# Performance work log

Measured on AMD Instinct MI355X. Metric: run time of the kernel, lower is better.

## Reference

```python
import jax, jax.numpy as jnp
import numpy as np

B = 16384  # batch size
DN = ('NCHW', 'OIHW', 'NCHW')


def maxpool2(x):
    # 2x2 max pool, stride 2, VALID (matches nn.MaxPool2d(2, 2))
    return jax.lax.reduce_window(x, -jnp.inf, jax.lax.max,
                                 (1, 1, 2, 2), (1, 1, 2, 2), 'VALID')


def setup_inputs() -> dict:
    key = jax.random.key(0)
    ks = jax.random.split(key, 7)
    return {
        'x': jax.random.normal(ks[0], (B, 1, 32, 32), jnp.float32),
        'w1': jax.random.normal(ks[1], (6, 1, 5, 5), jnp.float32) * 0.1,
        'w2': jax.random.normal(ks[2], (16, 6, 5, 5), jnp.float32) * 0.1,
        'fw1': jax.random.normal(ks[3], (120, 400), jnp.float32) * 0.05,
        'fw2': jax.random.normal(ks[4], (84, 120), jnp.float32) * 0.05,
        'fc3_w': jax.random.normal(ks[5], (10, 84), jnp.float32) * 0.1,
        'fc3_b': jax.random.normal(ks[6], (10,), jnp.float32) * 0.1,
    }


def reference(x, w1, w2, fw1, fw2, fc3_w, fc3_b):
    # conv1 (no bias in StdConv2D) -> relu -> pool
    h = jax.lax.conv_general_dilated(x, w1, (1, 1), 'VALID', dimension_numbers=DN)
    h = maxpool2(jax.nn.relu(h))                      # [B,6,14,14]
    # conv2 -> relu -> pool
    h = jax.lax.conv_general_dilated(h, w2, (1, 1), 'VALID', dimension_numbers=DN)
    h = maxpool2(jax.nn.relu(h))                      # [B,16,5,5]
    h = h.reshape(h.shape[0], 400)                    # channel-major flatten, as torch view
    # StdFC layers: x @ W.T, no bias
    h = jax.nn.relu(h @ fw1.T)                        # [B,120]
    h = jax.nn.relu(h @ fw2.T)                        # [B,84]
    logits = h @ fc3_w.T + fc3_b                      # nn.Linear fc3 with bias
    return jax.nn.softmax(logits, axis=1)
```

## Files before the change

kernel.cpp:

```cpp
#include <hip/hip_runtime.h>
#include <hip/hip_fp16.h>
#include <math.h>

#define TH 256

typedef __attribute__((ext_vector_type(8))) short short8;
typedef __attribute__((ext_vector_type(4))) float floatx4;

#define P1_S   0
#define X_S    9424
#define P2_S   9424
#define BT_S   12816
#define H1_S   12816
#define H2_S   13904
#define LOG_F  7368
#define W1B_U  7752
#define LDS_F  7904

static __device__ __forceinline__ unsigned short f2bf(float x) {
    union { float f; unsigned u; } v; v.f = x;
    return (unsigned short)((v.u + 0x7FFFu + ((v.u >> 16) & 1u)) >> 16);
}
static __device__ __forceinline__ __half2 uash2(unsigned u) {
    union { unsigned u; __half2 h; } v; v.u = u; return v.h;
}
static __device__ __forceinline__ unsigned bfpack(unsigned hi, unsigned lo) {
    return __builtin_amdgcn_perm(hi, lo, 0x07060302u);
}
static __device__ __forceinline__ short8 load_bf8t(const float* row, int kb, int K) {
    int b0 = (kb + 4 <= K) ? kb : (K - 8);
    int b1 = (kb + 8 <= K) ? (kb + 4) : (K - 8);
    uint4 w0 = *(const uint4*)(row + b0);
    uint4 w1 = *(const uint4*)(row + b1);
    union { int4 i; short8 s; } r;
    r.i.x = (int)bfpack(w0.y, w0.x);
    r.i.y = (int)bfpack(w0.w, w0.z);
    r.i.z = (int)bfpack(w1.y, w1.x);
    r.i.w = (int)bfpack(w1.w, w1.z);
    return r.s;
}

__global__ __launch_bounds__(TH) void lenet_kernel(
    const float* __restrict__ x,
    const float* __restrict__ w1,
    const float* __restrict__ w2g,
    const float* __restrict__ fw1,
    const float* __restrict__ fw2,
    const float* __restrict__ fc3w,
    const float* __restrict__ fc3b,
    float* __restrict__ out)
{
    __shared__ __align__(16) float sf[LDS_F];
    short* sh = (short*)sf;
    unsigned* su = (unsigned*)sf;
    const int* p1i = (const int*)sf;

    const int tid  = threadIdx.x;
    const int blk  = blockIdx.x;
    const int lane = tid & 63;
    const int wid  = tid >> 6;
    const int g    = lane >> 4;
    const int cn   = lane & 15;
    const int pr   = cn & 7;
    const int dyr  = cn >> 3;

    float4 xreg[3];
    {
        const float4* xg0 = (const float4*)(x + (size_t)blk * 8 * 1024);
        #pragma unroll
        for (int j = 0; j < 3; ++j) { int e = tid + j * TH; if (e < 768) xreg[j] = xg0[e]; }
    }
    for (int sub = 0; sub < 3; ++sub) {
        const int nimg = (sub < 2) ? 3 : 2;
        if (sub) __syncthreads();
        #pragma unroll
        for (int j = 0; j < 3; ++j) {
            int e = tid + j * TH;
            if (e < nimg * 256) {
                float4 v = xreg[j];
                int m = e >> 8, rem = e & 255;
                int y = rem >> 3, k4 = rem & 7;
                int off = X_S + m * 1090 + y * 34 + k4 * 4;
                *(__half2*)(sh + off)     = __floats2half2_rn(v.x, v.y);
                *(__half2*)(sh + off + 2) = __floats2half2_rn(v.z, v.w);
            }
        }
        if (sub == 0) {
            for (int e = tid; e < 150; e += TH) {
                __half h = __float2half(w1[e]);
                ((__half2*)(su + W1B_U))[e] = __half2half2(h);
            }
            for (int e = tid; e < 2560; e += TH) {
                int oc = e / 160, kk = e - oc * 160;
                int s = kk >> 5, r = kk & 31;
                float v = 0.f;
                if (r < 30) v = w2g[oc * 150 + (r % 6) * 25 + s * 5 + (r / 6)];
                sh[BT_S + oc * 168 + kk] = (short)f2bf(v);
            }
        }
        __syncthreads();

        if (sub < 2) {
            const int nimgn = (sub == 0) ? 3 : 2;
            const float4* xgn = (const float4*)(x + ((size_t)blk * 8 + (sub + 1) * 3) * 1024);
            #pragma unroll
            for (int j = 0; j < 3; ++j) { int e = tid + j * TH; if (e < nimgn * 256) xreg[j] = xgn[e]; }
        }

        const int ntask = nimg * 168;
        for (int t = tid; t < ntask; t += TH) {
            int m = t / 168, r = t - m * 168;
            int c = r % 6, q = r / 6;
            int i = q >> 1, hf = q & 1;
            const __half2* wb = (const __half2*)(su + W1B_U) + c * 25;
            const int xbase = X_S + m * 1090 + hf * 14;

            __half2 acc0[7], acc1[7];
            #pragma unroll
            for (int j = 0; j < 7; ++j) { acc0[j] = uash2(0u); acc1[j] = uash2(0u); }
            __half2 wprev[5];
            #pragma unroll
            for (int tt = 0; tt < 6; ++tt) {
                unsigned u[9];
                const unsigned* rp = (const unsigned*)(sh + xbase + (2 * i + tt) * 34);
                #pragma unroll
                for (int qq = 0; qq < 9; ++qq) u[qq] = rp[qq];
                __half2 p0[9], p1[8];
                #pragma unroll
                for (int qq = 0; qq < 9; ++qq) p0[qq] = uash2(u[qq]);
                #pragma unroll
                for (int qq = 0; qq < 8; ++qq)
                    p1[qq] = uash2(__builtin_amdgcn_perm(u[qq + 1], u[qq], 0x05040302u));

                if (tt < 5) {
                    __half2 wc[5];
                    #pragma unroll
                    for (int kx = 0; kx < 5; ++kx) wc[kx] = wb[tt * 5 + kx];
                    #pragma unroll
                    for (int j = 0; j < 7; ++j) {
                        acc0[j] = __hfma2(p0[j],     wc[0], acc0[j]);
                        acc0[j] = __hfma2(p1[j],     wc[1], acc0[j]);
                        acc0[j] = __hfma2(p0[j + 1], wc[2], acc0[j]);
                        acc0[j] = __hfma2(p1[j + 1], wc[3], acc0[j]);
                        acc0[j] = __hfma2(p0[j + 2], wc[4], acc0[j]);
                    }
                    if (tt >= 1) {
                        #pragma unroll
                        for (int j = 0; j < 7; ++j) {
                            acc1[j] = __hfma2(p0[j],     wprev[0], acc1[j]);
                            acc1[j] = __hfma2(p1[j],     wprev[1], acc1[j]);
                            acc1[j] = __hfma2(p0[j + 1], wprev[2], acc1[j]);
                            acc1[j] = __hfma2(p1[j + 1], wprev[3], acc1[j]);
                            acc1[j] = __hfma2(p0[j + 2], wprev[4], acc1[j]);
                        }
                    }
                    #pragma unroll
                    for (int kx = 0; kx < 5; ++kx) wprev[kx] = wc[kx];
                } else {
                    #pragma unroll
                    for (int j = 0; j < 7; ++j) {
                        acc1[j] = __hfma2(p0[j],     wprev[0], acc1[j]);
                        acc1[j] = __hfma2(p1[j],     wprev[1], acc1[j]);
                        acc1[j] = __hfma2(p0[j + 1], wprev[2], acc1[j]);
                        acc1[j] = __hfma2(p1[j + 1], wprev[3], acc1[j]);
                        acc1[j] = __hfma2(p0[j + 2], wprev[4], acc1[j]);
                    }
                }
            }
            int gi = sub * 3 + m;
            short* dst = sh + P1_S + gi * 1178 + i * 84 + hf * 42 + c;
            #pragma unroll
            for (int j = 0; j < 7; ++j) {
                float a0l = __half2float(__low2half(acc0[j]));
                float a0h = __half2float(__high2half(acc0[j]));
                float a1l = __half2float(__low2half(acc1[j]));
                float a1h = __half2float(__high2half(acc1[j]));
                float v = fmaxf(fmaxf(fmaxf(a0l, a0h), fmaxf(a1l, a1h)), 0.f);
                dst[j * 6] = (short)f2bf(v);
            }
        }
    }
    __syncthreads();

    {
        short8 Breg[5];
        #pragma unroll
        for (int s = 0; s < 5; ++s)
            Breg[s] = *(const short8*)(sh + BT_S + cn * 168 + s * 32 + 8 * g);

        for (int e = tid; e < 8 * 24; e += TH) {
            int im = e / 24;
            sh[P2_S + im * 424 + 400 + (e - im * 24)] = 0;
        }

        for (int w = wid; w < 25; w += 4) {
            int i = w / 5, jx = w - 5 * i;
            floatx4 a0 = {0.f,0.f,0.f,0.f}, a1 = {0.f,0.f,0.f,0.f};
            #pragma unroll
            for (int s = 0; s < 5; ++s) {
                #pragma unroll
                for (int dxp = 0; dxp < 2; ++dxp) {
                    int as = pr * 1178 + (2 * i + dyr + s) * 84 + (2 * jx + dxp) * 6 + 8 * g;
                    int ai = as >> 1;
                    union { int4 i4; short8 s8; } a;
                    a.i4.x = p1i[ai];     a.i4.y = p1i[ai + 1];
                    a.i4.z = p1i[ai + 2]; a.i4.w = p1i[ai + 3];
                    floatx4* acc = dxp == 0 ? &a0 : &a1;
                    *acc = __builtin_amdgcn_mfma_f32_16x16x32_bf16(a.s8, Breg[s], *acc, 0, 0, 0);
                }
            }
            #pragma unroll
            for (int rg = 0; rg < 4; ++rg) {
                float v = fmaxf(a0[rg], a1[rg]);
                v = fmaxf(v, __shfl_xor(v, 32));
                if (g < 2) {
                    int im = 4 * g + rg;
                    sh[P2_S + im * 424 + cn * 25 + i * 5 + jx] = (short)f2bf(fmaxf(v, 0.f));
                }
            }
        }
    }
    __syncthreads();

    {
        for (int e = tid; e < 8 * 16; e += TH) {
            int im = e >> 4;
            sh[H1_S + im * 136 + 120 + (e & 15)] = 0;
        }
        for (int nt = wid; nt < 8; nt += 4) {
            floatx4 acc = {0.f,0.f,0.f,0.f};
            int n = nt * 16 + cn;
            const float* wrow = fw1 + (size_t)(n < 120 ? n : 119) * 400;
            for (int ks = 0; ks < 13; ++ks) {
                int kb = ks * 32 + 8 * g;
                short8 b = load_bf8t(wrow, kb, 400);
                short8 a = *(const short8*)(sh + P2_S + pr * 424 + kb);
                acc = __builtin_amdgcn_mfma_f32_16x16x32_bf16(a, b, acc, 0, 0, 0);
            }
            if (g < 2 && n < 120) {
                #pragma unroll
                for (int rg = 0; rg < 4; ++rg)
                    sh[H1_S + (4 * g + rg) * 136 + n] = (short)f2bf(fmaxf(acc[rg], 0.f));
            }
        }
    }
    __syncthreads();

    {
        for (int e = tid; e < 8 * 20; e += TH) {
            int im = e / 20;
            sh[H2_S + im * 104 + 84 + (e - im * 20)] = 0;
        }
        for (int nt = wid; nt < 6; nt += 4) {
            floatx4 acc = {0.f,0.f,0.f,0.f};
            int n = nt * 16 + cn;
            const float* wrow = fw2 + (size_t)(n < 84 ? n : 83) * 120;
            for (int ks = 0; ks < 4; ++ks) {
                int kb = ks * 32 + 8 * g;
                short8 b = load_bf8t(wrow, kb, 120);
                short8 a = *(const short8*)(sh + H1_S + pr * 136 + kb);
                acc = __builtin_amdgcn_mfma_f32_16x16x32_bf16(a, b, acc, 0, 0, 0);
            }
            if (g < 2 && n < 84) {
                #pragma unroll
                for (int rg = 0; rg < 4; ++rg)
                    sh[H2_S + (4 * g + rg) * 104 + n] = (short)f2bf(fmaxf(acc[rg], 0.f));
            }
        }
    }
    __syncthreads();

    if (wid == 0) {
        floatx4 acc = {0.f,0.f,0.f,0.f};
        int n = cn;
        const float* wrow = fc3w + (size_t)(n < 10 ? n : 9) * 84;
        for (int ks = 0; ks < 3; ++ks) {
            int kb = ks * 32 + 8 * g;
            short8 b = load_bf8t(wrow, kb, 84);
            short8 a = *(const short8*)(sh + H2_S + pr * 104 + kb);
            acc = __builtin_amdgcn_mfma_f32_16x16x32_bf16(a, b, acc, 0, 0, 0);
        }
        if (g < 2 && n < 10) {
            float bias = fc3b[n];
            #pragma unroll
            for (int rg = 0; rg < 4; ++rg)
                sf[LOG_F + (4 * g + rg) * 12 + n] = acc[rg] + bias;
        }
    }
    __syncthreads();

    if (tid < 8) {
        const float* lg = sf + LOG_F + tid * 12;
        float mx = lg[0];
        #pragma unroll
        for (int n = 1; n < 10; ++n) mx = fmaxf(mx, lg[n]);
        float e[10]; float sum = 0.f;
        #pragma unroll
        for (int n = 0; n < 10; ++n) { e[n] = expf(lg[n] - mx); sum += e[n]; }
        float inv = 1.f / sum;
        float* op = out + ((size_t)blk * 8 + tid) * 10;
        #pragma unroll
        for (int n = 0; n < 10; ++n) op[n] = e[n] * inv;
    }
}

extern "C" void kernel_launch(void* const* d_in, const int* in_sizes, int n_in,
                              void* d_out, int out_size, void* d_ws, size_t ws_size,
                              hipStream_t stream) {
    const float* x    = (const float*)d_in[0];
    const float* w1   = (const float*)d_in[1];
    const float* w2   = (const float*)d_in[2];
    const float* fw1  = (const float*)d_in[3];
    const float* fw2  = (const float*)d_in[4];
    const float* fc3w = (const float*)d_in[5];
    const float* fc3b = (const float*)d_in[6];
    float* outp = (float*)d_out;

    dim3 grid(16384 / 8), block(TH);
    hipLaunchKernelGGL(lenet_kernel, grid, block, 0, stream,
                       x, w1, w2, fw1, fw2, fc3w, fc3b, outp);
}
```

Measured before the change: 82.24 us.

## Give each wavefront private conv1 staging for two images, removing block barriers

Replaces the three-pass block-wide conv1 stage (3/3/2 images per pass, each separated by __syncthreads) with a per-wavefront scheme: each of the 4 waves loads its own 2 images into registers, converts them into a private LDS region with a private copy of the conv1 weights, and computes its 336 conv1 tasks without block-level barriers. This removes the intermediate barriers and the serialized sub-pass structure, and loads all input up front. In exchange, LDS use rises (LDS_F grows from 7904 to 11624 floats), the w1 staging is replicated per wave, and 8 float4 registers per thread are held for the input, which may lower occupancy. Only 336 of 384 lane slots per wave do work in the last pass.

```diff
diff --git a/kernel.cpp b/kernel.cpp
--- a/kernel.cpp
+++ b/kernel.cpp
@@ -8,14 +8,16 @@
 typedef __attribute__((ext_vector_type(4))) float floatx4;
 
 #define P1_S   0
-#define X_S    9424
+#define X0_S   9424
+#define WVX    2184
 #define P2_S   9424
-#define BT_S   12816
 #define H1_S   12816
 #define H2_S   13904
 #define LOG_F  7368
-#define W1B_U  7752
-#define LDS_F  7904
+#define BT_S   18160
+#define W1U_0  10424
+#define W1U_W  300
+#define LDS_F  11624
 
 static __device__ __forceinline__ unsigned short f2bf(float x) {
     union { float f; unsigned u; } v; v.f = x;
@@ -64,56 +66,45 @@
     const int pr   = cn & 7;
     const int dyr  = cn >> 3;
 
-    float4 xreg[3];
+    const int Xw   = X0_S + wid * WVX;
+    const int W1u  = W1U_0 + wid * W1U_W;
+    const size_t imgbase = (size_t)blk * 8 + (size_t)wid * 2;
+
+    float4 xreg[8];
     {
-        const float4* xg0 = (const float4*)(x + (size_t)blk * 8 * 1024);
-        #pragma unroll
-        for (int j = 0; j < 3; ++j) { int e = tid + j * TH; if (e < 768) xreg[j] = xg0[e]; }
-    }
-    for (int sub = 0; sub < 3; ++sub) {
-        const int nimg = (sub < 2) ? 3 : 2;
-        if (sub) __syncthreads();
-        #pragma unroll
-        for (int j = 0; j < 3; ++j) {
-            int e = tid + j * TH;
-            if (e < nimg * 256) {
-                float4 v = xreg[j];
-                int m = e >> 8, rem = e & 255;
-                int y = rem >> 3, k4 = rem & 7;
-                int off = X_S + m * 1090 + y * 34 + k4 * 4;
-                *(__half2*)(sh + off)     = __floats2half2_rn(v.x, v.y);
-                *(__half2*)(sh + off + 2) = __floats2half2_rn(v.z, v.w);
-            }
-        }
-        if (sub == 0) {
-            for (int e = tid; e < 150; e += TH) {
-                __half h = __float2half(w1[e]);
-                ((__half2*)(su + W1B_U))[e] = __half2half2(h);
-            }
-            for (int e = tid; e < 2560; e += TH) {
-                int oc = e / 160, kk = e - oc * 160;
-                int s = kk >> 5, r = kk & 31;
-                float v = 0.f;
-                if (r < 30) v = w2g[oc * 150 + (r % 6) * 25 + s * 5 + (r / 6)];
-                sh[BT_S + oc * 168 + kk] = (short)f2bf(v);
-            }
-        }
-        __syncthreads();
-
-        if (sub < 2) {
-            const int nimgn = (sub == 0) ? 3 : 2;
-            const float4* xgn = (const float4*)(x + ((size_t)blk * 8 + (sub + 1) * 3) * 1024);
-            #pragma unroll
-            for (int j = 0; j < 3; ++j) { int e = tid + j * TH; if (e < nimgn * 256) xreg[j] = xgn[e]; }
-        }
-
-        const int ntask = nimg * 168;
-        for (int t = tid; t < ntask; t += TH) {
-            int m = t / 168, r = t - m * 168;
+        const float4* xg = (const float4*)(x + imgbase * 1024);
+        #pragma unroll
+        for (int j = 0; j < 8; ++j) xreg[j] = xg[lane + j * 64];
+    }
+
+    for (int e = tid; e < 2560; e += TH) {
+        int oc = e / 160, kk = e - oc * 160;
+        int s = kk >> 5, r = kk & 31;
+        float v = 0.f;
+        if (r < 30) v = w2g[oc * 150 + (r % 6) * 25 + s * 5 + (r / 6)];
+        sh[BT_S + oc * 168 + kk] = (short)f2bf(v);
+    }
+    for (int e = lane; e < 150; e += 64)
+        ((__half2*)(su + W1u))[e] = __half2half2(__float2half(w1[e]));
+
+    #pragma unroll
+    for (int j = 0; j < 8; ++j) {
+        int e = lane + (j & 3) * 64;
+        float4 v = xreg[j];
+        int y = e >> 3, k4 = e & 7;
+        int off = Xw + (j >> 2) * 1090 + y * 34 + k4 * 4;
+        *(__half2*)(sh + off)     = __floats2half2_rn(v.x, v.y);
+        *(__half2*)(sh + off + 2) = __floats2half2_rn(v.z, v.w);
+    }
+
+    for (int p = 0; p < 6; ++p) {
+        int t = p * 64 + lane;
+        if (t < 336) {
+            int img = t / 168, r = t - img * 168;
             int c = r % 6, q = r / 6;
             int i = q >> 1, hf = q & 1;
-            const __half2* wb = (const __half2*)(su + W1B_U) + c * 25;
-            const int xbase = X_S + m * 1090 + hf * 14;
+            const __half2* wb = (const __half2*)(su + W1u) + c * 25;
+            const int xbase = Xw + img * 1090 + hf * 14;
 
             __half2 acc0[7], acc1[7];
             #pragma unroll
@@ -167,7 +158,7 @@
                     }
                 }
             }
-            int gi = sub * 3 + m;
+            int gi = wid * 2 + img;
             short* dst = sh + P1_S + gi * 1178 + i * 84 + hf * 42 + c;
             #pragma unroll
             for (int j = 0; j < 7; ++j) {
```

Result: slower. 89.73 us (+9.1%).

## Use 512 threads, stage all eight images at once, switch MFMA to fp16

Applied to the files above, without the earlier changes.

Doubles the block to 512 threads and loads all eight images into LDS in one pass, which removes the three-substep conv1 loop and its extra barriers. Replaces the bf16 MFMA path with fp16 (cvt_pkrtz packing for weights, half stores for activations), dropping the manual bf16 rounding. Each wave now handles one FC1 tile and one FC2 tile. LDS use rises and each block holds more waves, so occupancy may drop; fp16 range and precision differ from bf16.

```diff
diff --git a/kernel.cpp b/kernel.cpp
--- a/kernel.cpp
+++ b/kernel.cpp
@@ -2,42 +2,36 @@
 #include <hip/hip_fp16.h>
 #include <math.h>
 
-#define TH 256
-
-typedef __attribute__((ext_vector_type(8))) short short8;
+#define TH 512
+
+typedef __attribute__((ext_vector_type(8))) _Float16 half8;
 typedef __attribute__((ext_vector_type(4))) float floatx4;
 
 #define P1_S   0
 #define X_S    9424
 #define P2_S   9424
-#define BT_S   12816
-#define H1_S   12816
-#define H2_S   13904
-#define LOG_F  7368
-#define W1B_U  7752
-#define LDS_F  7904
-
-static __device__ __forceinline__ unsigned short f2bf(float x) {
-    union { float f; unsigned u; } v; v.f = x;
-    return (unsigned short)((v.u + 0x7FFFu + ((v.u >> 16) & 1u)) >> 16);
-}
+#define BT_S   18144
+#define H1_S   18144
+#define H2_S   19232
+#define LOG_F  10032
+#define W1_U   10416
+#define LDS_F  10566
+
 static __device__ __forceinline__ __half2 uash2(unsigned u) {
     union { unsigned u; __half2 h; } v; v.u = u; return v.h;
 }
-static __device__ __forceinline__ unsigned bfpack(unsigned hi, unsigned lo) {
-    return __builtin_amdgcn_perm(hi, lo, 0x07060302u);
-}
-static __device__ __forceinline__ short8 load_bf8t(const float* row, int kb, int K) {
+static __device__ __forceinline__ half8 load_h8(const float* row, int kb, int K) {
     int b0 = (kb + 4 <= K) ? kb : (K - 8);
     int b1 = (kb + 8 <= K) ? (kb + 4) : (K - 8);
-    uint4 w0 = *(const uint4*)(row + b0);
-    uint4 w1 = *(const uint4*)(row + b1);
-    union { int4 i; short8 s; } r;
-    r.i.x = (int)bfpack(w0.y, w0.x);
-    r.i.y = (int)bfpack(w0.w, w0.z);
-    r.i.z = (int)bfpack(w1.y, w1.x);
-    r.i.w = (int)bfpack(w1.w, w1.z);
-    return r.s;
+    float4 w0 = *(const float4*)(row + b0);
+    float4 w1 = *(const float4*)(row + b1);
+    union { unsigned u[4]; half8 v; } r;
+    union { __fp16 __attribute__((ext_vector_type(2))) h; unsigned u; } c;
+    c.h = __builtin_amdgcn_cvt_pkrtz(w0.x, w0.y); r.u[0] = c.u;
+    c.h = __builtin_amdgcn_cvt_pkrtz(w0.z, w0.w); r.u[1] = c.u;
+    c.h = __builtin_amdgcn_cvt_pkrtz(w1.x, w1.y); r.u[2] = c.u;
+    c.h = __builtin_amdgcn_cvt_pkrtz(w1.z, w1.w); r.u[3] = c.u;
+    return r.v;
 }
 
 __global__ __launch_bounds__(TH) void lenet_kernel(
@@ -52,6 +46,7 @@
 {
     __shared__ __align__(16) float sf[LDS_F];
     short* sh = (short*)sf;
+    __half* hp = (__half*)sf;
     unsigned* su = (unsigned*)sf;
     const int* p1i = (const int*)sf;
 
@@ -64,99 +59,71 @@
     const int pr   = cn & 7;
     const int dyr  = cn >> 3;
 
-    float4 xreg[3];
     {
-        const float4* xg0 = (const float4*)(x + (size_t)blk * 8 * 1024);
-        #pragma unroll
-        for (int j = 0; j < 3; ++j) { int e = tid + j * TH; if (e < 768) xreg[j] = xg0[e]; }
-    }
-    for (int sub = 0; sub < 3; ++sub) {
-        const int nimg = (sub < 2) ? 3 : 2;
-        if (sub) __syncthreads();
-        #pragma unroll
-        for (int j = 0; j < 3; ++j) {
+        float4 xreg[4];
+        const float4* xg = (const float4*)(x + (size_t)blk * 8 * 1024);
+        #pragma unroll
+        for (int j = 0; j < 4; ++j) xreg[j] = xg[tid + j * TH];
+
+        for (int e = tid; e < 150; e += TH)
+            ((__half2*)(su + W1_U))[e] = __half2half2(__float2half(w1[e]));
+        for (int e = tid; e < 2560; e += TH) {
+            int oc = e / 160, kk = e - oc * 160;
+            int s = kk >> 5, r = kk & 31;
+            float v = 0.f;
+            if (r < 30) v = w2g[oc * 150 + (r % 6) * 25 + s * 5 + (r / 6)];
+            hp[BT_S + oc * 168 + kk] = __float2half(v);
+        }
+        #pragma unroll
+        for (int j = 0; j < 4; ++j) {
             int e = tid + j * TH;
-            if (e < nimg * 256) {
-                float4 v = xreg[j];
-                int m = e >> 8, rem = e & 255;
-                int y = rem >> 3, k4 = rem & 7;
-                int off = X_S + m * 1090 + y * 34 + k4 * 4;
-                *(__half2*)(sh + off)     = __floats2half2_rn(v.x, v.y);
-                *(__half2*)(sh + off + 2) = __floats2half2_rn(v.z, v.w);
-            }
-        }
-        if (sub == 0) {
-            for (int e = tid; e < 150; e += TH) {
-                __half h = __float2half(w1[e]);
-                ((__half2*)(su + W1B_U))[e] = __half2half2(h);
-            }
-            for (int e = tid; e < 2560; e += TH) {
-                int oc = e / 160, kk = e - oc * 160;
-                int s = kk >> 5, r = kk & 31;
-                float v = 0.f;
-                if (r < 30) v = w2g[oc * 150 + (r % 6) * 25 + s * 5 + (r / 6)];
-                sh[BT_S + oc * 168 + kk] = (short)f2bf(v);
-            }
-        }
-        __syncthreads();
-
-        if (sub < 2) {
-            const int nimgn = (sub == 0) ? 3 : 2;
-            const float4* xgn = (const float4*)(x + ((size_t)blk * 8 + (sub + 1) * 3) * 1024);
-            #pragma unroll
-            for (int j = 0; j < 3; ++j) { int e = tid + j * TH; if (e < nimgn * 256) xreg[j] = xgn[e]; }
-        }
-
-        const int ntask = nimg * 168;
-        for (int t = tid; t < ntask; t += TH) {
-            int m = t / 168, r = t - m * 168;
-            int c = r % 6, q = r / 6;
-            int i = q >> 1, hf = q & 1;
-            const __half2* wb = (const __half2*)(su + W1B_U) + c * 25;
-            const int xbase = X_S + m * 1090 + hf * 14;
-
-            __half2 acc0[7], acc1[7];
-            #pragma unroll
-            for (int j = 0; j < 7; ++j) { acc0[j] = uash2(0u); acc1[j] = uash2(0u); }
-            __half2 wprev[5];
-            #pragma unroll
-            for (int tt = 0; tt < 6; ++tt) {
-                unsigned u[9];
-                const unsigned* rp = (const unsigned*)(sh + xbase + (2 * i + tt) * 34);
-                #pragma unroll
-                for (int qq = 0; qq < 9; ++qq) u[qq] = rp[qq];
-                __half2 p0[9], p1[8];
-                #pragma unroll
-                for (int qq = 0; qq < 9; ++qq) p0[qq] = uash2(u[qq]);
-                #pragma unroll
-                for (int qq = 0; qq < 8; ++qq)
-                    p1[qq] = uash2(__builtin_amdgcn_perm(u[qq + 1], u[qq], 0x05040302u));
-
-                if (tt < 5) {
-                    __half2 wc[5];
-                    #pragma unroll
-                    for (int kx = 0; kx < 5; ++kx) wc[kx] = wb[tt * 5 + kx];
-                    #pragma unroll
-                    for (int j = 0; j < 7; ++j) {
-                        acc0[j] = __hfma2(p0[j],     wc[0], acc0[j]);
-                        acc0[j] = __hfma2(p1[j],     wc[1], acc0[j]);
-                        acc0[j] = __hfma2(p0[j + 1], wc[2], acc0[j]);
-                        acc0[j] = __hfma2(p1[j + 1], wc[3], acc0[j]);
-                        acc0[j] = __hfma2(p0[j + 2], wc[4], acc0[j]);
-                    }
-                    if (tt >= 1) {
-                        #pragma unroll
-                        for (int j = 0; j < 7; ++j) {
-                            acc1[j] = __hfma2(p0[j],     wprev[0], acc1[j]);
-                            acc1[j] = __hfma2(p1[j],     wprev[1], acc1[j]);
-                            acc1[j] = __hfma2(p0[j + 1], wprev[2], acc1[j]);
-                            acc1[j] = __hfma2(p1[j + 1], wprev[3], acc1[j]);
-                            acc1[j] = __hfma2(p0[j + 2], wprev[4], acc1[j]);
-                        }
-                    }
-                    #pragma unroll
-                    for (int kx = 0; kx < 5; ++kx) wprev[kx] = wc[kx];
-                } else {
+            int m = e >> 8, rem = e & 255;
+            int y = rem >> 3, k4 = rem & 7;
+            int off = X_S + m * 1090 + y * 34 + k4 * 4;
+            float4 v = xreg[j];
+            *(__half2*)(sh + off)     = __floats2half2_rn(v.x, v.y);
+            *(__half2*)(sh + off + 2) = __floats2half2_rn(v.z, v.w);
+        }
+    }
+    __syncthreads();
+
+    for (int t = tid; t < 1344; t += TH) {
+        int m = t / 168, r = t - m * 168;
+        int c = r % 6, q = r / 6;
+        int i = q >> 1, hf = q & 1;
+        const __half2* wb = (const __half2*)(su + W1_U) + c * 25;
+        const int xbase = X_S + m * 1090 + hf * 14;
+
+        __half2 acc0[7], acc1[7];
+        #pragma unroll
+        for (int j = 0; j < 7; ++j) { acc0[j] = uash2(0u); acc1[j] = uash2(0u); }
+        __half2 wprev[5];
+        #pragma unroll
+        for (int tt = 0; tt < 6; ++tt) {
+            unsigned u[9];
+            const unsigned* rp = (const unsigned*)(sh + xbase + (2 * i + tt) * 34);
+            #pragma unroll
+            for (int qq = 0; qq < 9; ++qq) u[qq] = rp[qq];
+            __half2 p0[9], p1[8];
+            #pragma unroll
+            for (int qq = 0; qq < 9; ++qq) p0[qq] = uash2(u[qq]);
+            #pragma unroll
+            for (int qq = 0; qq < 8; ++qq)
+                p1[qq] = uash2(__builtin_amdgcn_perm(u[qq + 1], u[qq], 0x05040302u));
+
+            if (tt < 5) {
+                __half2 wc[5];
+                #pragma unroll
+                for (int kx = 0; kx < 5; ++kx) wc[kx] = wb[tt * 5 + kx];
+                #pragma unroll
+                for (int j = 0; j < 7; ++j) {
+                    acc0[j] = __hfma2(p0[j],     wc[0], acc0[j]);
+                    acc0[j] = __hfma2(p1[j],     wc[1], acc0[j]);
+                    acc0[j] = __hfma2(p0[j + 1], wc[2], acc0[j]);
+                    acc0[j] = __hfma2(p1[j + 1], wc[3], acc0[j]);
+                    acc0[j] = __hfma2(p0[j + 2], wc[4], acc0[j]);
+                }
+                if (tt >= 1) {
                     #pragma unroll
                     for (int j = 0; j < 7; ++j) {
                         acc1[j] = __hfma2(p0[j],     wprev[0], acc1[j]);
@@ -166,34 +133,44 @@
                         acc1[j] = __hfma2(p0[j + 2], wprev[4], acc1[j]);
                     }
                 }
+                #pragma unroll
+                for (int kx = 0; kx < 5; ++kx) wprev[kx] = wc[kx];
+            } else {
+                #pragma unroll
+                for (int j = 0; j < 7; ++j) {
+                    acc1[j] = __hfma2(p0[j],     wprev[0], acc1[j]);
+                    acc1[j] = __hfma2(p1[j],     wprev[1], acc1[j]);
+                    acc1[j] = __hfma2(p0[j + 1], wprev[2], acc1[j]);
+                    acc1[j] = __hfma2(p1[j + 1], wprev[3], acc1[j]);
+                    acc1[j] = __hfma2(p0[j + 2], wprev[4], acc1[j]);
+                }
             }
-            int gi = sub * 3 + m;
-            short* dst = sh + P1_S + gi * 1178 + i * 84 + hf * 42 + c;
-            #pragma unroll
-            for (int j = 0; j < 7; ++j) {
-                float a0l = __half2float(__low2half(acc0[j]));
-                float a0h = __half2float(__high2half(acc0[j]));
-                float a1l = __half2float(__low2half(acc1[j]));
-                float a1h = __half2float(__high2half(acc1[j]));
-                float v = fmaxf(fmaxf(fmaxf(a0l, a0h), fmaxf(a1l, a1h)), 0.f);
-                dst[j * 6] = (short)f2bf(v);
-            }
+        }
+        __half* dst = hp + P1_S + m * 1178 + i * 84 + hf * 42 + c;
+        #pragma unroll
+        for (int j = 0; j < 7; ++j) {
+            float a0l = __half2float(__low2half(acc0[j]));
+            float a0h = __half2float(__high2half(acc0[j]));
+            float a1l = __half2float(__low2half(acc1[j]));
+            float a1h = __half2float(__high2half(acc1[j]));
+            float v = fmaxf(fmaxf(fmaxf(a0l, a0h), fmaxf(a1l, a1h)), 0.f);
+            dst[j * 6] = __float2half(v);
         }
     }
     __syncthreads();
 
     {
-        short8 Breg[5];
+        half8 Breg[5];
         #pragma unroll
         for (int s = 0; s < 5; ++s)
-            Breg[s] = *(const short8*)(sh + BT_S + cn * 168 + s * 32 + 8 * g);
-
-        for (int e = tid; e < 8 * 24; e += TH) {
-            int im = e / 24;
-            sh[P2_S + im * 424 + 400 + (e - im * 24)] = 0;
-        }
-
-        for (int w = wid; w < 25; w += 4) {
+            Breg[s] = *(const half8*)(sh + BT_S + cn * 168 + s * 32 + 8 * g);
+
+        if (tid < 192) {
+            int im = tid / 24;
+            sh[P2_S + im * 424 + 400 + (tid - im * 24)] = 0;
+        }
+
+        for (int w = wid; w < 25; w += 8) {
             int i = w / 5, jx = w - 5 * i;
             floatx4 a0 = {0.f,0.f,0.f,0.f}, a1 = {0.f,0.f,0.f,0.f};
             #pragma unroll
@@ -202,11 +179,11 @@
                 for (int dxp = 0; dxp < 2; ++dxp) {
                     int as = pr * 1178 + (2 * i + dyr + s) * 84 + (2 * jx + dxp) * 6 + 8 * g;
                     int ai = as >> 1;
-                    union { int4 i4; short8 s8; } a;
+                    union { int4 i4; half8 h8; } a;
                     a.i4.x = p1i[ai];     a.i4.y = p1i[ai + 1];
                     a.i4.z = p1i[ai + 2]; a.i4.w = p1i[ai + 3];
                     floatx4* acc = dxp == 0 ? &a0 : &a1;
-                    *acc = __builtin_amdgcn_mfma_f32_16x16x32_bf16(a.s8, Breg[s], *acc, 0, 0, 0);
+                    *acc = __builtin_amdgcn_mfma_f32_16x16x32_f16(a.h8, Breg[s], *acc, 0, 0, 0);
                 }
             }
             #pragma unroll
@@ -215,7 +192,7 @@
                 v = fmaxf(v, __shfl_xor(v, 32));
                 if (g < 2) {
                     int im = 4 * g + rg;
-                    sh[P2_S + im * 424 + cn * 25 + i * 5 + jx] = (short)f2bf(fmaxf(v, 0.f));
+                    hp[P2_S + im * 424 + cn * 25 + i * 5 + jx] = __float2half(fmaxf(v, 0.f));
                 }
             }
         }
@@ -223,49 +200,44 @@
     __syncthreads();
 
     {
-        for (int e = tid; e < 8 * 16; e += TH) {
-            int im = e >> 4;
-            sh[H1_S + im * 136 + 120 + (e & 15)] = 0;
-        }
-        for (int nt = wid; nt < 8; nt += 4) {
-            floatx4 acc = {0.f,0.f,0.f,0.f};
-            int n = nt * 16 + cn;
-            const float* wrow = fw1 + (size_t)(n < 120 ? n : 119) * 400;
-            for (int ks = 0; ks < 13; ++ks) {
-                int kb = ks * 32 + 8 * g;
-                short8 b = load_bf8t(wrow, kb, 400);
-                short8 a = *(const short8*)(sh + P2_S + pr * 424 + kb);
-                acc = __builtin_amdgcn_mfma_f32_16x16x32_bf16(a, b, acc, 0, 0, 0);
-            }
-            if (g < 2 && n < 120) {
-                #pragma unroll
-                for (int rg = 0; rg < 4; ++rg)
-                    sh[H1_S + (4 * g + rg) * 136 + n] = (short)f2bf(fmaxf(acc[rg], 0.f));
-            }
-        }
-    }
-    __syncthreads();
-
-    {
-        for (int e = tid; e < 8 * 20; e += TH) {
-            int im = e / 20;
+        if (tid < 128)
+            sh[H1_S + (tid >> 4) * 136 + 120 + (tid & 15)] = 0;
+        if (tid >= 128 && tid < 288) {
+            int e = tid - 128, im = e / 20;
             sh[H2_S + im * 104 + 84 + (e - im * 20)] = 0;
         }
-        for (int nt = wid; nt < 6; nt += 4) {
-            floatx4 acc = {0.f,0.f,0.f,0.f};
-            int n = nt * 16 + cn;
-            const float* wrow = fw2 + (size_t)(n < 84 ? n : 83) * 120;
-            for (int ks = 0; ks < 4; ++ks) {
-                int kb = ks * 32 + 8 * g;
-                short8 b = load_bf8t(wrow, kb, 120);
-                short8 a = *(const short8*)(sh + H1_S + pr * 136 + kb);
-                acc = __builtin_amdgcn_mfma_f32_16x16x32_bf16(a, b, acc, 0, 0, 0);
-            }
-            if (g < 2 && n < 84) {
-                #pragma unroll
-                for (int rg = 0; rg < 4; ++rg)
-                    sh[H2_S + (4 * g + rg) * 104 + n] = (short)f2bf(fmaxf(acc[rg], 0.f));
-            }
+        int nt = wid;
+        floatx4 acc = {0.f,0.f,0.f,0.f};
+        int n = nt * 16 + cn;
+        const float* wrow = fw1 + (size_t)(n < 120 ? n : 119) * 400;
+        for (int ks = 0; ks < 13; ++ks) {
+            int kb = ks * 32 + 8 * g;
+            half8 b = load_h8(wrow, kb, 400);
+            half8 a = *(const half8*)(sh + P2_S + pr * 424 + kb);
+            acc = __builtin_amdgcn_mfma_f32_16x16x32_f16(a, b, acc, 0, 0, 0);
+        }
+        if (g < 2 && n < 120) {
+            #pragma unroll
+            for (int rg = 0; rg < 4; ++rg)
+                hp[H1_S + (4 * g + rg) * 136 + n] = __float2half(fmaxf(acc[rg], 0.f));
+        }
+    }
+    __syncthreads();
+
+    if (wid < 6) {
+        floatx4 acc = {0.f,0.f,0.f,0.f};
+        int n = wid * 16 + cn;
+        const float* wrow = fw2 + (size_t)(n < 84 ? n : 83) * 120;
+        for (int ks = 0; ks < 4; ++ks) {
+            int kb = ks * 32 + 8 * g;
+            half8 b = load_h8(wrow, kb, 120);
+            half8 a = *(const half8*)(sh + H1_S + pr * 136 + kb);
+            acc = __builtin_amdgcn_mfma_f32_16x16x32_f16(a, b, acc, 0, 0, 0);
+        }
+        if (g < 2 && n < 84) {
+            #pragma unroll
+            for (int rg = 0; rg < 4; ++rg)
+                hp[H2_S + (4 * g + rg) * 104 + n] = __float2half(fmaxf(acc[rg], 0.f));
         }
     }
     __syncthreads();
@@ -276,9 +248,9 @@
         const float* wrow = fc3w + (size_t)(n < 10 ? n : 9) * 84;
         for (int ks = 0; ks < 3; ++ks) {
             int kb = ks * 32 + 8 * g;
-            short8 b = load_bf8t(wrow, kb, 84);
-            short8 a = *(const short8*)(sh + H2_S + pr * 104 + kb);
-            acc = __builtin_amdgcn_mfma_f32_16x16x32_bf16(a, b, acc, 0, 0, 0);
+            half8 b = load_h8(wrow, kb, 84);
+            half8 a = *(const half8*)(sh + H2_S + pr * 104 + kb);
+            acc = __builtin_amdgcn_mfma_f32_16x16x32_f16(a, b, acc, 0, 0, 0);
         }
         if (g < 2 && n < 10) {
             float bias = fc3b[n];
```

New measurement: 89.25 us. 1.09x slower.
